# Optimization experiments

Measured on AMD Instinct MI355X. Metric: run time of the kernel, lower is better.

Reference implementation:

```python
import jax, jax.numpy as jnp
import numpy as np

EPS = 1e-5
NEG_SLOPE = 0.2

def _bn(x, gamma, beta):
    # BatchNorm1d in training mode: stats over (batch, length) per channel. x: [B,C,N]
    m = jnp.mean(x, axis=(0, 2), keepdims=True)
    v = jnp.mean((x - m) ** 2, axis=(0, 2), keepdims=True)  # biased variance
    return (x - m) * jax.lax.rsqrt(v + EPS) * gamma[None, :, None] + beta[None, :, None]

def setup_inputs() -> dict:
    key = jax.random.key(0)
    ks = jax.random.split(key, 7)
    B, C, N, H = 32, 64, 2048, 128
    s = 1.0 / np.sqrt(C)
    return {
        "x": jax.random.normal(ks[0], (B, C, N), dtype=jnp.float32),
        "wq": jax.random.normal(ks[1], (C, C), dtype=jnp.float32) * s,
        "wk": jax.random.normal(ks[2], (C, C), dtype=jnp.float32) * s,
        "wv": jax.random.normal(ks[3], (C, C), dtype=jnp.float32) * s,
        "w_ff1": jax.random.normal(ks[4], (H, C), dtype=jnp.float32) * s,
        "w_ff2": jax.random.normal(ks[5], (C, H), dtype=jnp.float32) * (1.0 / np.sqrt(H)),
        "bn1_gamma": jnp.ones((C,), dtype=jnp.float32),
        "bn1_beta": jnp.zeros((C,), dtype=jnp.float32),
        "bn2_gamma": jnp.ones((C,), dtype=jnp.float32),
        "bn2_beta": jnp.zeros((C,), dtype=jnp.float32),
    }

def reference(x, wq, wk, wv, w_ff1, w_ff2, bn1_gamma, bn1_beta, bn2_gamma, bn2_beta):
    # x: [B, C, N]; 1x1 convs are per-point channel matmuls
    C = x.shape[1]
    q = jnp.einsum('oc,bcn->bno', wq, x)          # [B,N,C]
    k = jnp.einsum('oc,bcn->bon', wk, x)          # [B,C,N]
    v = jnp.einsum('oc,bcn->bno', wv, x)          # [B,N,C] (v^T)
    energy = jnp.einsum('bnc,bcm->bnm', q, k)     # [B,N,N]
    attention = jax.nn.softmax(energy / jnp.sqrt(jnp.float32(C)), axis=-1)
    x_r = jnp.einsum('bnm,bmc->bcn', attention, v)  # [B,C,N]
    h = _bn(x + x_r, bn1_gamma, bn1_beta)
    ff = jnp.einsum('hc,bcn->bhn', w_ff1, h)      # [B,H,N]
    ff = jnp.where(ff >= 0, ff, NEG_SLOPE * ff)   # LeakyReLU(0.2)
    ff = jnp.einsum('ch,bhn->bcn', w_ff2, ff)     # [B,C,N]
    return _bn(h + ff, bn2_gamma, bn2_beta)
```

## Files before the change

kernel.cpp:

```cpp
#include <hip/hip_runtime.h>

#define B_ 32
#define C_ 64
#define N_ 2048
#define H_ 128
#define MSHIFT 12.0f

typedef unsigned short u16;
typedef unsigned int u32;
typedef float f32x4 __attribute__((ext_vector_type(4)));
typedef float f32x16 __attribute__((ext_vector_type(16)));
typedef __bf16 bf16x8 __attribute__((ext_vector_type(8)));
typedef __bf16 bf16x4 __attribute__((ext_vector_type(4)));
typedef unsigned short u16x4 __attribute__((ext_vector_type(4)));
typedef unsigned int u32x4v __attribute__((ext_vector_type(4)));

#define MFMA(a, b, c) __builtin_amdgcn_mfma_f32_16x16x32_bf16(a, b, c, 0, 0, 0)
#define MFMA32(a, b, c) __builtin_amdgcn_mfma_f32_32x32x16_bf16(a, b, c, 0, 0, 0)
#define EXP2(x) __builtin_amdgcn_exp2f(x)
#define LOG2E 1.44269504088896f

__device__ __forceinline__ int swz(int row, int cb) { return row * 128 + (cb ^ ((row & 7) << 4)); }
__device__ __forceinline__ int swz256(int row, int cb) { return row * 256 + (cb ^ ((row & 7) << 4)); }

__device__ __forceinline__ float b2f(u16 v) {
    union { u32 u; float f; } x; x.u = ((u32)v) << 16; return x.f;
}

__device__ __forceinline__ u32 cvtpk(float lo, float hi) {
    u32 r;
    asm("v_cvt_pk_bf16_f32 %0, %1, %2" : "=v"(r) : "v"(lo), "v"(hi));
    return r;
}

__device__ __forceinline__ bf16x8 pfrag(float p0, float p1, float p2, float p3,
                                        float p4, float p5, float p6, float p7) {
    u32 x1 = cvtpk(p0, p1), x2 = cvtpk(p2, p3);
    u32 y1 = cvtpk(p4, p5), y2 = cvtpk(p6, p7);
    asm volatile("v_permlane32_swap_b32 %0, %1" : "+v"(x1), "+v"(y1));
    asm volatile("v_permlane32_swap_b32 %0, %1" : "+v"(x2), "+v"(y2));
    u32x4v d; d[0] = x1; d[1] = x2; d[2] = y1; d[3] = y2;
    return __builtin_bit_cast(bf16x8, d);
}

__device__ __forceinline__ bf16x8 cvt8(const float* p, float s) {
    f32x4 a = *(const f32x4*)p, b = *(const f32x4*)(p + 4);
    bf16x8 o;
    o[0] = (__bf16)(a[0] * s); o[1] = (__bf16)(a[1] * s);
    o[2] = (__bf16)(a[2] * s); o[3] = (__bf16)(a[3] * s);
    o[4] = (__bf16)(b[0] * s); o[5] = (__bf16)(b[1] * s);
    o[6] = (__bf16)(b[2] * s); o[7] = (__bf16)(b[3] * s);
    return o;
}

__global__ __launch_bounds__(256) void qkv_k(
    const float* __restrict__ x,
    const float* __restrict__ wq, const float* __restrict__ wk, const float* __restrict__ wv,
    const float* __restrict__ w1, const float* __restrict__ w2,
    u16* __restrict__ Qg, u16* __restrict__ Kg, u16* __restrict__ Vg,
    u16* __restrict__ w1b, u16* __restrict__ w2b)
{
    const int b = blockIdx.y, nt = blockIdx.x, t = threadIdx.x;
    const int lane = t & 63, wave = t >> 6, g = lane >> 4, r16 = lane & 15;
    __shared__ __align__(16) u16 xT[128 * 64];
    const int n0 = nt * 128;

    bf16x8 wqf[4][2], wkf[4][2], wvf[4][2];
#pragma unroll
    for (int jt = 0; jt < 4; ++jt)
#pragma unroll
        for (int kc = 0; kc < 2; ++kc) {
            const int ro = (r16 + 16 * jt) * 64 + 8 * g + 32 * kc;
            wqf[jt][kc] = cvt8(wq + ro, 0.125f * LOG2E);
            wkf[jt][kc] = cvt8(wk + ro, 1.0f);
            wvf[jt][kc] = cvt8(wv + ro, 1.0f);
        }

    {
        int c = t >> 5;
        const int nn = (t & 31) * 4;
#pragma unroll
        for (int pass = 0; pass < 8; ++pass, c += 8) {
            f32x4 v = *(const f32x4*)&x[(size_t)(b * 64 + c) * 2048 + n0 + nn];
#pragma unroll
            for (int j = 0; j < 4; ++j)
                xT[swz(nn + j, 2 * c) >> 1] = __builtin_bit_cast(u16, (__bf16)v[j]);
        }
    }
    if (b == 0 && nt == 0) {
        for (int i = t; i < H_ * C_; i += 256) w1b[i] = __builtin_bit_cast(u16, (__bf16)w1[i]);
        for (int i = t; i < C_ * H_; i += 256) w2b[i] = __builtin_bit_cast(u16, (__bf16)w2[i]);
    }
    __syncthreads();

#pragma unroll
    for (int p = 0; p < 2; ++p) {
        const int nt16 = wave * 2 + p;
        bf16x8 xa[2];
#pragma unroll
        for (int kc = 0; kc < 2; ++kc)
            xa[kc] = *(const bf16x8*)&xT[swz(nt16 * 16 + r16, 16 * g + 64 * kc) >> 1];
#pragma unroll
        for (int jt = 0; jt < 4; ++jt) {
            f32x4 aq = {0.f, 0.f, 0.f, 0.f}, ak = {0.f, 0.f, 0.f, 0.f};
            aq = MFMA(wqf[jt][0], xa[0], aq); aq = MFMA(wqf[jt][1], xa[1], aq);
            ak = MFMA(wkf[jt][0], xa[0], ak); ak = MFMA(wkf[jt][1], xa[1], ak);
            bf16x4 qk, kk;
#pragma unroll
            for (int r = 0; r < 4; ++r) { qk[r] = (__bf16)aq[r]; kk[r] = (__bf16)ak[r]; }
            const size_t ro = (size_t)(b * 2048 + n0 + nt16 * 16 + r16) * 64 + 16 * jt + 4 * g;
            *(bf16x4*)&Qg[ro] = qk;
            *(bf16x4*)&Kg[ro] = kk;
        }
#pragma unroll
        for (int it = 0; it < 4; ++it) {
            f32x4 av = {0.f, 0.f, 0.f, 0.f};
            av = MFMA(xa[0], wvf[it][0], av);
            av = MFMA(xa[1], wvf[it][1], av);
            bf16x4 vk;
#pragma unroll
            for (int r = 0; r < 4; ++r) vk[r] = (__bf16)av[r];
            *(bf16x4*)&Vg[(size_t)(b * 64 + 16 * it + r16) * 2048 + n0 + nt16 * 16 + 4 * g] = vk;
        }
    }
}

__global__ __launch_bounds__(256) void attn_k(
    const u16* __restrict__ Qg, const u16* __restrict__ Kg, const u16* __restrict__ Vg,
    const float* __restrict__ x, u16* __restrict__ yb,
    float* __restrict__ ps, float* __restrict__ pq)
{
    const int t = threadIdx.x;
    const int lane = t & 63, wave = t >> 6, q = lane & 31, hi = lane >> 5;
    const int L = blockIdx.x;
    const int xcd = L & 7, slot = L >> 3;
    const int b = xcd * 4 + (slot >> 3);
    const int qt = slot & 7;

    __shared__ __align__(16) u16 Lds16[16384];
    char* lds = (char*)Lds16;

    const int n0 = qt * 256 + wave * 64;

    bf16x8 qf[2][4];
#pragma unroll
    for (int u = 0; u < 2; ++u) {
        const u16* qrow = Qg + (size_t)(b * 2048 + n0 + 32 * u + q) * 64 + 8 * hi;
#pragma unroll
        for (int kc = 0; kc < 4; ++kc)
            qf[u][kc] = *(const bf16x8*)(qrow + 16 * kc);
    }

    f32x16 acc[2][2];
#pragma unroll
    for (int u = 0; u < 2; ++u)
#pragma unroll
        for (int ct = 0; ct < 2; ++ct)
#pragma unroll
            for (int r = 0; r < 16; ++r) acc[u][ct][r] = 0.f;
    float lp[2] = {0.f, 0.f};

    const char* Kgb = (const char*)Kg + (size_t)b * 2048 * 128;
    const char* Vgb = (const char*)Vg + (size_t)b * 64 * 4096;
    const int srcxor = (((lane & 7) ^ (lane >> 3)) << 4);
    const int rowb = wave * 16 + (lane >> 3);

    auto stage = [&](int kvt, int buf) {
#pragma unroll
        for (int j = 0; j < 2; ++j) {
            const char* gk = Kgb + (size_t)(kvt * 64 + rowb + 8 * j) * 128 + srcxor;
            const char* gv = Vgb + (size_t)(rowb + 8 * j) * 4096 + kvt * 128 + srcxor;
            char* lk = lds + buf * 8192 + (wave * 2 + j) * 1024;
            __builtin_amdgcn_global_load_lds(
                (const __attribute__((address_space(1))) void*)gk,
                (__attribute__((address_space(3))) void*)lk, 16, 0, 0);
            __builtin_amdgcn_global_load_lds(
                (const __attribute__((address_space(1))) void*)gv,
                (__attribute__((address_space(3))) void*)(lk + 16384), 16, 0, 0);
        }
    };

    auto tile = [&](int kvt, int buf) {
        __syncthreads();
        if (kvt + 1 < 32) stage(kvt + 1, buf ^ 1);
        const char* Kc = lds + buf * 8192;
        const char* Vc = Kc + 16384;

        bf16x8 kf[8], vf[8];
#pragma unroll
        for (int i = 0; i < 8; ++i)
            kf[i] = *(const bf16x8*)(Kc + swz(32 * (i >> 2) + q, 32 * (i & 3) + 16 * hi));
#pragma unroll
        for (int i = 0; i < 8; ++i)
            vf[i] = *(const bf16x8*)(Vc + swz(32 * (i >> 2) + q, 32 * (i & 3) + 16 * hi));

        f32x16 st[2][2];
        __builtin_amdgcn_s_setprio(1);
#pragma unroll
        for (int u = 0; u < 2; ++u)
#pragma unroll
            for (int it = 0; it < 2; ++it) {
                f32x16 a;
#pragma unroll
                for (int r = 0; r < 16; ++r) a[r] = -MSHIFT;
#pragma unroll
                for (int kc = 0; kc < 4; ++kc)
                    a = MFMA32(kf[4 * it + kc], qf[u][kc], a);
                st[u][it] = a;
            }
        __builtin_amdgcn_s_setprio(0);

#pragma unroll
        for (int u = 0; u < 2; ++u) {
#pragma unroll
            for (int it = 0; it < 2; ++it)
#pragma unroll
                for (int r = 0; r < 16; ++r) st[u][it][r] = EXP2(st[u][it][r]);
            float ls = 0.f;
#pragma unroll
            for (int it = 0; it < 2; ++it) {
                float a0 = (st[u][it][0] + st[u][it][1]) + (st[u][it][2] + st[u][it][3]);
                float a1 = (st[u][it][4] + st[u][it][5]) + (st[u][it][6] + st[u][it][7]);
                float a2 = (st[u][it][8] + st[u][it][9]) + (st[u][it][10] + st[u][it][11]);
                float a3 = (st[u][it][12] + st[u][it][13]) + (st[u][it][14] + st[u][it][15]);
                ls += (a0 + a1) + (a2 + a3);
            }
            lp[u] += ls;
            bf16x8 pf0 = pfrag(st[u][0][0], st[u][0][1], st[u][0][2], st[u][0][3],
                               st[u][0][4], st[u][0][5], st[u][0][6], st[u][0][7]);
            bf16x8 pf1 = pfrag(st[u][0][8], st[u][0][9], st[u][0][10], st[u][0][11],
                               st[u][0][12], st[u][0][13], st[u][0][14], st[u][0][15]);
            bf16x8 pf2 = pfrag(st[u][1][0], st[u][1][1], st[u][1][2], st[u][1][3],
                               st[u][1][4], st[u][1][5], st[u][1][6], st[u][1][7]);
            bf16x8 pf3 = pfrag(st[u][1][8], st[u][1][9], st[u][1][10], st[u][1][11],
                               st[u][1][12], st[u][1][13], st[u][1][14], st[u][1][15]);
            __builtin_amdgcn_s_setprio(1);
#pragma unroll
            for (int ct = 0; ct < 2; ++ct) {
                acc[u][ct] = MFMA32(vf[4 * ct + 0], pf0, acc[u][ct]);
                acc[u][ct] = MFMA32(vf[4 * ct + 1], pf1, acc[u][ct]);
                acc[u][ct] = MFMA32(vf[4 * ct + 2], pf2, acc[u][ct]);
                acc[u][ct] = MFMA32(vf[4 * ct + 3], pf3, acc[u][ct]);
            }
            __builtin_amdgcn_s_setprio(0);
        }
    };

    stage(0, 0);
#pragma unroll 1
    for (int kvt = 0; kvt < 32; kvt += 2) {
        tile(kvt, 0);
        tile(kvt + 1, 1);
    }

    float inv[2];
#pragma unroll
    for (int u = 0; u < 2; ++u) {
        const float l = lp[u] + __shfl_xor(lp[u], 32, 64);
        inv[u] = 1.0f / l;
    }
    float sv[2][16], qv[2][16];
#pragma unroll
    for (int ct = 0; ct < 2; ++ct)
#pragma unroll
        for (int r = 0; r < 16; ++r) { sv[ct][r] = 0.f; qv[ct][r] = 0.f; }
#pragma unroll
    for (int u = 0; u < 2; ++u) {
        const int n = n0 + 32 * u + q;
#pragma unroll
        for (int ct = 0; ct < 2; ++ct)
#pragma unroll
            for (int grp = 0; grp < 4; ++grp) {
                bf16x4 ov;
#pragma unroll
                for (int j = 0; j < 4; ++j) {
                    const int r = 4 * grp + j;
                    const int c = 32 * ct + j + 8 * grp + 4 * hi;
                    const float o = acc[u][ct][r] * inv[u] + x[(size_t)(b * 64 + c) * 2048 + n];
                    sv[ct][r] += o;
                    qv[ct][r] += o * o;
                    ov[j] = (__bf16)o;
                }
                *(bf16x4*)&yb[(size_t)(b * 2048 + n) * 64 + 32 * ct + 8 * grp + 4 * hi] = ov;
            }
    }
#pragma unroll
    for (int d = 1; d <= 16; d <<= 1)
#pragma unroll
        for (int ct = 0; ct < 2; ++ct)
#pragma unroll
            for (int r = 0; r < 16; ++r) {
                sv[ct][r] += __shfl_xor(sv[ct][r], d, 64);
                qv[ct][r] += __shfl_xor(qv[ct][r], d, 64);
            }
    __syncthreads();
    float* sb = (float*)lds;
    if (q == 0) {
#pragma unroll
        for (int ct = 0; ct < 2; ++ct)
#pragma unroll
            for (int r = 0; r < 16; ++r) {
                const int c = 32 * ct + (r & 3) + 8 * (r >> 2) + 4 * hi;
                sb[wave * 64 + c] = sv[ct][r];
                sb[256 + wave * 64 + c] = qv[ct][r];
            }
    }
    __syncthreads();
    if (t < 64) {
        ps[L * 64 + t] = sb[t] + sb[64 + t] + sb[128 + t] + sb[192 + t];
        pq[L * 64 + t] = sb[256 + t] + sb[320 + t] + sb[384 + t] + sb[448 + t];
    }
}

__global__ __launch_bounds__(256) void finalize_k(
    const float* __restrict__ psum, const float* __restrict__ psq,
    const float* __restrict__ gamma, const float* __restrict__ beta,
    float* __restrict__ ss, int nblk)
{
    const int c = blockIdx.x, t = threadIdx.x;
    const int lane = t & 63, wave = t >> 6;
    float s = 0.f, q = 0.f;
    for (int bl = t; bl < nblk; bl += 256) {
        s += psum[bl * 64 + c];
        q += psq[bl * 64 + c];
    }
#pragma unroll
    for (int d = 1; d <= 32; d <<= 1) {
        s += __shfl_xor(s, d, 64);
        q += __shfl_xor(q, d, 64);
    }
    __shared__ float ls[4], lq[4];
    if (lane == 0) { ls[wave] = s; lq[wave] = q; }
    __syncthreads();
    if (t == 0) {
        s = ls[0] + ls[1] + ls[2] + ls[3];
        q = lq[0] + lq[1] + lq[2] + lq[3];
        const float mean = s * (1.0f / 65536.0f);
        const float var  = q * (1.0f / 65536.0f) - mean * mean;
        const float sc   = rsqrtf(var + 1e-5f) * gamma[c];
        ss[c] = sc;
        ss[64 + c] = beta[c] - mean * sc;
    }
}

__global__ __launch_bounds__(256) void ff_k(
    const u16* __restrict__ y, const float* __restrict__ ss1,
    const u16* __restrict__ w1b, const u16* __restrict__ w2b,
    u16* __restrict__ zb, float* __restrict__ ps, float* __restrict__ pq)
{
    const int b = blockIdx.y, nt = blockIdx.x, t = threadIdx.x;
    const int lane = t & 63, wave = t >> 6, g = lane >> 4, r16 = lane & 15;
    const int L = blockIdx.y * gridDim.x + blockIdx.x;
    __shared__ __align__(16) u16 hT[64 * 64];
    __shared__ __align__(16) float hf[64 * 68];
    __shared__ __align__(16) u16 pb[4][16 * 128];
    __shared__ float sc1[64], sh1[64];
    if (t < 64) { sc1[t] = ss1[t]; sh1[t] = ss1[64 + t]; }
    __syncthreads();
    const int n0 = nt * 64;
    {
        const int i = t >> 2, c0 = (t & 3) * 16;
        u16 yb16[16] __attribute__((aligned(16)));
        *(uint4*)&yb16[0] = *(const uint4*)&y[(size_t)(b * 2048 + n0 + i) * 64 + c0];
        *(uint4*)&yb16[8] = *(const uint4*)&y[(size_t)(b * 2048 + n0 + i) * 64 + c0 + 8];
        u16 hb[16] __attribute__((aligned(16)));
#pragma unroll
        for (int q4 = 0; q4 < 4; ++q4) {
            f32x4 hv;
#pragma unroll
            for (int j = 0; j < 4; ++j) {
                const int c = c0 + 4 * q4 + j;
                hv[j] = b2f(yb16[4 * q4 + j]) * sc1[c] + sh1[c];
                hb[4 * q4 + j] = __builtin_bit_cast(u16, (__bf16)hv[j]);
            }
            *(f32x4*)&hf[i * 68 + c0 + 4 * q4] = hv;
        }
        *(uint4*)&hT[swz(i, 2 * c0) >> 1]      = *(const uint4*)&hb[0];
        *(uint4*)&hT[swz(i, 2 * c0 + 16) >> 1] = *(const uint4*)&hb[8];
    }
    __syncthreads();

    bf16x8 ha[2];
#pragma unroll
    for (int kc = 0; kc < 2; ++kc)
        ha[kc] = *(const bf16x8*)&hT[swz(wave * 16 + r16, 16 * g + 64 * kc) >> 1];
#pragma unroll
    for (int it = 0; it < 8; ++it) {
        f32x4 a = {0.f, 0.f, 0.f, 0.f};
#pragma unroll
        for (int kc = 0; kc < 2; ++kc) {
            bf16x8 w1f = *(const bf16x8*)&w1b[(r16 + 16 * it) * 64 + 8 * g + 32 * kc];
            a = MFMA(w1f, ha[kc], a);
        }
        u16x4 pk;
#pragma unroll
        for (int r = 0; r < 4; ++r) {
            const float rv = a[r] >= 0.f ? a[r] : 0.2f * a[r];
            pk[r] = __builtin_bit_cast(u16, (__bf16)rv);
        }
        *(u16x4*)&pb[wave][swz256(r16, 2 * (16 * it + 4 * g)) >> 1] = pk;
    }
    bf16x8 pa[4];
#pragma unroll
    for (int kc = 0; kc < 4; ++kc)
        pa[kc] = *(const bf16x8*)&pb[wave][swz256(r16, 16 * g + 64 * kc) >> 1];
    const int nl = wave * 16 + r16;
    float sv[4][4], qv[4][4];
#pragma unroll
    for (int jt = 0; jt < 4; ++jt) {
        f32x4 a = {0.f, 0.f, 0.f, 0.f};
#pragma unroll
        for (int kc = 0; kc < 4; ++kc) {
            bf16x8 w2f = *(const bf16x8*)&w2b[(r16 + 16 * jt) * 128 + 8 * g + 32 * kc];
            a = MFMA(w2f, pa[kc], a);
        }
        f32x4 h4 = *(const f32x4*)&hf[nl * 68 + 16 * jt + 4 * g];
        bf16x4 zk;
#pragma unroll
        for (int r = 0; r < 4; ++r) {
            a[r] += h4[r];
            sv[jt][r] = a[r];
            qv[jt][r] = a[r] * a[r];
            zk[r] = (__bf16)a[r];
        }
        *(bf16x4*)&zb[(size_t)(b * 2048 + n0 + nl) * 64 + 16 * jt + 4 * g] = zk;
    }
#pragma unroll
    for (int d = 1; d <= 8; d <<= 1)
#pragma unroll
        for (int jt = 0; jt < 4; ++jt)
#pragma unroll
            for (int r = 0; r < 4; ++r) {
                sv[jt][r] += __shfl_xor(sv[jt][r], d, 64);
                qv[jt][r] += __shfl_xor(qv[jt][r], d, 64);
            }
    __syncthreads();
    float* sb = (float*)&pb[0][0];
    if (r16 == 0) {
#pragma unroll
        for (int jt = 0; jt < 4; ++jt)
#pragma unroll
            for (int r = 0; r < 4; ++r) {
                const int c = 16 * jt + 4 * g + r;
                sb[wave * 64 + c] = sv[jt][r];
                sb[256 + wave * 64 + c] = qv[jt][r];
            }
    }
    __syncthreads();
    if (t < 64) {
        ps[L * 64 + t] = sb[t] + sb[64 + t] + sb[128 + t] + sb[192 + t];
        pq[L * 64 + t] = sb[256 + t] + sb[320 + t] + sb[384 + t] + sb[448 + t];
    }
}

__global__ __launch_bounds__(256) void bnout_k(
    const u16* __restrict__ zb, const float* __restrict__ ss2, float* __restrict__ out)
{
    const int b = blockIdx.y, nt = blockIdx.x, t = threadIdx.x;
    __shared__ float tile[64 * 68];
    __shared__ float sc2[64], sh2[64];
    if (t < 64) { sc2[t] = ss2[t]; sh2[t] = ss2[64 + t]; }
    __syncthreads();
    const int n0 = nt * 64;
    {
        const int i = t >> 2, c0 = (t & 3) * 16;
        u16 zb16[16] __attribute__((aligned(16)));
        *(uint4*)&zb16[0] = *(const uint4*)&zb[(size_t)(b * 2048 + n0 + i) * 64 + c0];
        *(uint4*)&zb16[8] = *(const uint4*)&zb[(size_t)(b * 2048 + n0 + i) * 64 + c0 + 8];
#pragma unroll
        for (int q4 = 0; q4 < 4; ++q4) {
            f32x4 tv;
#pragma unroll
            for (int j = 0; j < 4; ++j) {
                const int c = c0 + 4 * q4 + j;
                tv[j] = b2f(zb16[4 * q4 + j]) * sc2[c] + sh2[c];
            }
            *(f32x4*)&tile[i * 68 + c0 + 4 * q4] = tv;
        }
    }
    __syncthreads();
    {
        const int c = t >> 2, j0 = (t & 3) * 16;
#pragma unroll
        for (int q4 = 0; q4 < 4; ++q4) {
            f32x4 ov;
#pragma unroll
            for (int j = 0; j < 4; ++j)
                ov[j] = tile[(j0 + 4 * q4 + j) * 68 + c];
            *(f32x4*)&out[(size_t)(b * 64 + c) * 2048 + n0 + j0 + 4 * q4] = ov;
        }
    }
}

extern "C" void kernel_launch(void* const* d_in, const int* in_sizes, int n_in,
                              void* d_out, int out_size, void* d_ws, size_t ws_size,
                              hipStream_t stream)
{
    const float* x   = (const float*)d_in[0];
    const float* wq  = (const float*)d_in[1];
    const float* wk  = (const float*)d_in[2];
    const float* wv  = (const float*)d_in[3];
    const float* w1  = (const float*)d_in[4];
    const float* w2  = (const float*)d_in[5];
    const float* g1  = (const float*)d_in[6];
    const float* be1 = (const float*)d_in[7];
    const float* g2  = (const float*)d_in[8];
    const float* be2 = (const float*)d_in[9];
    float* out = (float*)d_out;

    char* w = (char*)d_ws;
    u16* Qg = (u16*)w;   w += (size_t)B_ * N_ * C_ * 2;
    u16* Kg = (u16*)w;   w += (size_t)B_ * N_ * C_ * 2;
    u16* Vg = (u16*)w;   w += (size_t)B_ * N_ * C_ * 2;
    u16* yb = (u16*)w;   w += (size_t)B_ * N_ * C_ * 2;
    u16* zb = (u16*)w;   w += (size_t)B_ * N_ * C_ * 2;
    u16* w1b = (u16*)w;  w += (size_t)H_ * C_ * 2;
    u16* w2b = (u16*)w;  w += (size_t)C_ * H_ * 2;
    float* ps1 = (float*)w; w += 1024 * 64 * 4;
    float* pq1 = (float*)w; w += 1024 * 64 * 4;
    float* ps2 = (float*)w; w += 1024 * 64 * 4;
    float* pq2 = (float*)w; w += 1024 * 64 * 4;
    float* ss1 = (float*)w; w += 128 * 4;
    float* ss2 = (float*)w; w += 128 * 4;

    const dim3 blk(256);
    hipLaunchKernelGGL(qkv_k,   dim3(16, 32), blk, 0, stream, x, wq, wk, wv, w1, w2, Qg, Kg, Vg, w1b, w2b);
    hipLaunchKernelGGL(attn_k,  dim3(256),    blk, 0, stream, Qg, Kg, Vg, x, yb, ps1, pq1);
    hipLaunchKernelGGL(finalize_k, dim3(64),  blk, 0, stream, ps1, pq1, g1, be1, ss1, 256);
    hipLaunchKernelGGL(ff_k,    dim3(32, 32), blk, 0, stream, yb, ss1, w1b, w2b, zb, ps2, pq2);
    hipLaunchKernelGGL(finalize_k, dim3(64),  blk, 0, stream, ps2, pq2, g2, be2, ss2, 1024);
    hipLaunchKernelGGL(bnout_k, dim3(32, 32), blk, 0, stream, zb, ss2, out);
}
```

Measured before the change: 126.8 us.

## Split KV range across two wave groups per attention block and merge in LDS

The attention kernel now launches 512 threads per block, with two groups of four waves each processing half of the key/value sequence for the same query tile. After the loop, the second group writes its partial accumulators and row sums to LDS and the first group adds them before the normalization, residual and statistics epilogue. This doubles the waves per CU to better hide memory and MFMA latency. In exchange it adds an LDS reduction step, a larger shared-memory footprint, and a tighter register budget from the 512-thread launch bound.

After: 140.4 us. 10.7% more time.

```diff
diff --git a/kernel.cpp b/kernel.cpp
--- a/kernel.cpp
+++ b/kernel.cpp
@@ -125,22 +125,25 @@
     }
 }
 
-__global__ __launch_bounds__(256) void attn_k(
+__global__ __launch_bounds__(512, 2) void attn_k(
     const u16* __restrict__ Qg, const u16* __restrict__ Kg, const u16* __restrict__ Vg,
     const float* __restrict__ x, u16* __restrict__ yb,
     float* __restrict__ ps, float* __restrict__ pq)
 {
     const int t = threadIdx.x;
-    const int lane = t & 63, wave = t >> 6, q = lane & 31, hi = lane >> 5;
+    const int lane = t & 63, wave = t >> 6;
+    const int wq4 = wave & 3, half = wave >> 2;
+    const int q = lane & 31, hi = lane >> 5;
     const int L = blockIdx.x;
     const int xcd = L & 7, slot = L >> 3;
     const int b = xcd * 4 + (slot >> 3);
     const int qt = slot & 7;
 
-    __shared__ __align__(16) u16 Lds16[16384];
+    __shared__ __align__(16) u16 Lds16[33792];
     char* lds = (char*)Lds16;
-
-    const int n0 = qt * 256 + wave * 64;
+    char* ldsh = lds + half * 32768;
+
+    const int n0 = qt * 256 + wq4 * 64;
 
     bf16x8 qf[2][4];
 #pragma unroll
@@ -160,17 +163,17 @@
             for (int r = 0; r < 16; ++r) acc[u][ct][r] = 0.f;
     float lp[2] = {0.f, 0.f};
 
-    const char* Kgb = (const char*)Kg + (size_t)b * 2048 * 128;
-    const char* Vgb = (const char*)Vg + (size_t)b * 64 * 4096;
+    const char* Kgb = (const char*)Kg + (size_t)b * 2048 * 128 + (size_t)half * 1024 * 128;
+    const char* Vgb = (const char*)Vg + (size_t)b * 64 * 4096 + half * 2048;
     const int srcxor = (((lane & 7) ^ (lane >> 3)) << 4);
-    const int rowb = wave * 16 + (lane >> 3);
+    const int rowb = wq4 * 16 + (lane >> 3);
 
     auto stage = [&](int kvt, int buf) {
 #pragma unroll
         for (int j = 0; j < 2; ++j) {
             const char* gk = Kgb + (size_t)(kvt * 64 + rowb + 8 * j) * 128 + srcxor;
             const char* gv = Vgb + (size_t)(rowb + 8 * j) * 4096 + kvt * 128 + srcxor;
-            char* lk = lds + buf * 8192 + (wave * 2 + j) * 1024;
+            char* lk = ldsh + buf * 8192 + (wq4 * 2 + j) * 1024;
             __builtin_amdgcn_global_load_lds(
                 (const __attribute__((address_space(1))) void*)gk,
                 (__attribute__((address_space(3))) void*)lk, 16, 0, 0);
@@ -182,8 +185,8 @@
 
     auto tile = [&](int kvt, int buf) {
         __syncthreads();
-        if (kvt + 1 < 32) stage(kvt + 1, buf ^ 1);
-        const char* Kc = lds + buf * 8192;
+        if (kvt + 1 < 16) stage(kvt + 1, buf ^ 1);
+        const char* Kc = ldsh + buf * 8192;
         const char* Vc = Kc + 16384;
 
         bf16x8 kf[8], vf[8];
@@ -248,9 +251,44 @@
 
     stage(0, 0);
 #pragma unroll 1
-    for (int kvt = 0; kvt < 32; kvt += 2) {
+    for (int kvt = 0; kvt < 16; kvt += 2) {
         tile(kvt, 0);
         tile(kvt + 1, 1);
+    }
+
+    __syncthreads();
+    float* lpb = (float*)(lds + 65536);
+    if (half == 1) {
+        char* base = lds + wq4 * 16384 + lane * 256;
+#pragma unroll
+        for (int u = 0; u < 2; ++u)
+#pragma unroll
+            for (int ct = 0; ct < 2; ++ct)
+#pragma unroll
+                for (int p = 0; p < 4; ++p) {
+                    f32x4 v4;
+#pragma unroll
+                    for (int j = 0; j < 4; ++j) v4[j] = acc[u][ct][4 * p + j];
+                    *(f32x4*)(base + (u * 2 + ct) * 64 + p * 16) = v4;
+                }
+        lpb[(wq4 * 64 + lane) * 2 + 0] = lp[0];
+        lpb[(wq4 * 64 + lane) * 2 + 1] = lp[1];
+    }
+    __syncthreads();
+    if (half == 0) {
+        const char* base = lds + wq4 * 16384 + lane * 256;
+#pragma unroll
+        for (int u = 0; u < 2; ++u)
+#pragma unroll
+            for (int ct = 0; ct < 2; ++ct)
+#pragma unroll
+                for (int p = 0; p < 4; ++p) {
+                    f32x4 v4 = *(const f32x4*)(base + (u * 2 + ct) * 64 + p * 16);
+#pragma unroll
+                    for (int j = 0; j < 4; ++j) acc[u][ct][4 * p + j] += v4[j];
+                }
+        lp[0] += lpb[(wq4 * 64 + lane) * 2 + 0];
+        lp[1] += lpb[(wq4 * 64 + lane) * 2 + 1];
     }
 
     float inv[2];
@@ -264,25 +302,27 @@
     for (int ct = 0; ct < 2; ++ct)
 #pragma unroll
         for (int r = 0; r < 16; ++r) { sv[ct][r] = 0.f; qv[ct][r] = 0.f; }
-#pragma unroll
-    for (int u = 0; u < 2; ++u) {
-        const int n = n0 + 32 * u + q;
-#pragma unroll
-        for (int ct = 0; ct < 2; ++ct)
-#pragma unroll
-            for (int grp = 0; grp < 4; ++grp) {
-                bf16x4 ov;
-#pragma unroll
-                for (int j = 0; j < 4; ++j) {
-                    const int r = 4 * grp + j;
-                    const int c = 32 * ct + j + 8 * grp + 4 * hi;
-                    const float o = acc[u][ct][r] * inv[u] + x[(size_t)(b * 64 + c) * 2048 + n];
-                    sv[ct][r] += o;
-                    qv[ct][r] += o * o;
-                    ov[j] = (__bf16)o;
+    if (half == 0) {
+#pragma unroll
+        for (int u = 0; u < 2; ++u) {
+            const int n = n0 + 32 * u + q;
+#pragma unroll
+            for (int ct = 0; ct < 2; ++ct)
+#pragma unroll
+                for (int grp = 0; grp < 4; ++grp) {
+                    bf16x4 ov;
+#pragma unroll
+                    for (int j = 0; j < 4; ++j) {
+                        const int r = 4 * grp + j;
+                        const int c = 32 * ct + j + 8 * grp + 4 * hi;
+                        const float o = acc[u][ct][r] * inv[u] + x[(size_t)(b * 64 + c) * 2048 + n];
+                        sv[ct][r] += o;
+                        qv[ct][r] += o * o;
+                        ov[j] = (__bf16)o;
+                    }
+                    *(bf16x4*)&yb[(size_t)(b * 2048 + n) * 64 + 32 * ct + 8 * grp + 4 * hi] = ov;
                 }
-                *(bf16x4*)&yb[(size_t)(b * 2048 + n) * 64 + 32 * ct + 8 * grp + 4 * hi] = ov;
-            }
+        }
     }
 #pragma unroll
     for (int d = 1; d <= 16; d <<= 1)
@@ -302,13 +342,16 @@
             for (int r = 0; r < 16; ++r) {
                 const int c = 32 * ct + (r & 3) + 8 * (r >> 2) + 4 * hi;
                 sb[wave * 64 + c] = sv[ct][r];
-                sb[256 + wave * 64 + c] = qv[ct][r];
+                sb[512 + wave * 64 + c] = qv[ct][r];
             }
     }
     __syncthreads();
     if (t < 64) {
-        ps[L * 64 + t] = sb[t] + sb[64 + t] + sb[128 + t] + sb[192 + t];
-        pq[L * 64 + t] = sb[256 + t] + sb[320 + t] + sb[384 + t] + sb[448 + t];
+        float s = 0.f, qq = 0.f;
+#pragma unroll
+        for (int w = 0; w < 8; ++w) { s += sb[w * 64 + t]; qq += sb[512 + w * 64 + t]; }
+        ps[L * 64 + t] = s;
+        pq[L * 64 + t] = qq;
     }
 }
 
@@ -523,11 +566,10 @@
     float* ss1 = (float*)w; w += 128 * 4;
     float* ss2 = (float*)w; w += 128 * 4;
 
-    const dim3 blk(256);
-    hipLaunchKernelGGL(qkv_k,   dim3(16, 32), blk, 0, stream, x, wq, wk, wv, w1, w2, Qg, Kg, Vg, w1b, w2b);
-    hipLaunchKernelGGL(attn_k,  dim3(256),    blk, 0, stream, Qg, Kg, Vg, x, yb, ps1, pq1);
-    hipLaunchKernelGGL(finalize_k, dim3(64),  blk, 0, stream, ps1, pq1, g1, be1, ss1, 256);
-    hipLaunchKernelGGL(ff_k,    dim3(32, 32), blk, 0, stream, yb, ss1, w1b, w2b, zb, ps2, pq2);
-    hipLaunchKernelGGL(finalize_k, dim3(64),  blk, 0, stream, ps2, pq2, g2, be2, ss2, 1024);
-    hipLaunchKernelGGL(bnout_k, dim3(32, 32), blk, 0, stream, zb, ss2, out);
-}
+    hipLaunchKernelGGL(qkv_k,   dim3(16, 32), dim3(256), 0, stream, x, wq, wk, wv, w1, w2, Qg, Kg, Vg, w1b, w2b);
+    hipLaunchKernelGGL(attn_k,  dim3(256),    dim3(512), 0, stream, Qg, Kg, Vg, x, yb, ps1, pq1);
+    hipLaunchKernelGGL(finalize_k, dim3(64),  dim3(256), 0, stream, ps1, pq1, g1, be1, ss1, 256);
+    hipLaunchKernelGGL(ff_k,    dim3(32, 32), dim3(256), 0, stream, yb, ss1, w1b, w2b, zb, ps2, pq2);
+    hipLaunchKernelGGL(finalize_k, dim3(64),  dim3(256), 0, stream, ps2, pq2, g2, be2, ss2, 1024);
+    hipLaunchKernelGGL(bnout_k, dim3(32, 32), dim3(256), 0, stream, zb, ss2, out);
+}
```
